# Performance work log

Hardware: AMD Instinct MI355X
Metric: run time of the kernel (lower is better)

Reference implementation:

```python
import jax, jax.numpy as jnp
import numpy as np

B, N, D, H = 8, 512, 512, 16
DH = D // H          # 32
HH = H // 2          # 8
DEG = 16
E = B * N * DEG      # 65536
LOG2 = float(np.log(2.0))


def _lin(key, fan_in, fan_out):
    k1, k2 = jax.random.split(key)
    s = 1.0 / np.sqrt(fan_in)
    W = jax.random.uniform(k1, (fan_in, fan_out), jnp.float32, -s, s)
    b = jax.random.uniform(k2, (fan_out,), jnp.float32, -s, s)
    return W, b


def setup_inputs() -> dict:
    key = jax.random.key(0)
    ks = jax.random.split(key, 12)
    inp = {}
    inp["key"] = jax.random.normal(ks[0], (B, N, D), jnp.float32)
    inp["value"] = jax.random.normal(ks[1], (B, N, D), jnp.float32)
    inp["query"] = jax.random.normal(ks[2], (B, N, D), jnp.float32)
    inp["mask"] = jnp.zeros((B, N, N), bool)
    inp["edge_feature"] = jax.random.normal(ks[3], (E, D), jnp.float32)
    # deterministic, collision-free (b,i,j) edge index: DEG neighbors per node
    inp["pair_b"] = jnp.repeat(jnp.arange(B, dtype=jnp.int32), N * DEG)
    i_idx = jnp.tile(jnp.repeat(jnp.arange(N, dtype=jnp.int32), DEG), B)
    inp["pair_i"] = i_idx
    inp["pair_j"] = (i_idx + 1 + jnp.tile(jnp.arange(DEG, dtype=jnp.int32), B * N)) % N
    inp["Wq"], inp["bq"] = _lin(ks[4], D, D)
    inp["Wk"], inp["bk"] = _lin(ks[5], D, D)
    inp["Wv"], inp["bv"] = _lin(ks[6], D, D)
    inp["Wo"], inp["bo"] = _lin(ks[7], D, D)
    inp["We1"], inp["be1"] = _lin(ks[8], D, D)
    inp["We2"], inp["be2"] = _lin(ks[9], D, D // 2)
    inp["Wu1"], inp["bu1"] = _lin(ks[10], 2 * D, D)
    inp["Wu2"], inp["bu2"] = _lin(ks[11], D, D)
    return inp


def reference(key, value, query, mask, edge_feature, pair_b, pair_i, pair_j,
              Wq, bq, Wk, bk, Wv, bv, Wo, bo,
              We1, be1, We2, be2, Wu1, bu1, Wu2, bu2):
    scale = 1.0 / np.sqrt(DH)

    def shape(x):  # (B,N,D) -> (B,H,N,DH)
        return x.reshape(B, N, H, DH).transpose(0, 2, 1, 3)

    k = shape(key @ Wk + bk)
    q = shape(query @ Wq + bq)
    v = shape(value @ Wv + bv)

    # ---- local, edge-indexed half (upper HH heads) ----
    ef = jax.nn.softplus(edge_feature @ We1 + be1) - LOG2  # SSP
    ef = (ef @ We2 + be2).reshape(E, HH, DH)
    k_loc = k[pair_b, HH:, pair_j] * ef                    # (E,HH,DH)
    q_loc = q[pair_b, HH:, pair_i] * scale                 # (E,HH,DH)
    scores_local = jnp.einsum('ehd,ehd->eh', q_loc, k_loc)  # (E,HH)
    score_expand = jnp.full((B, N, N, HH), -jnp.inf, scores_local.dtype)
    score_expand = score_expand.at[pair_b, pair_i, pair_j].set(scores_local)
    score_expand = score_expand.transpose(0, 3, 1, 2)      # (B,HH,N,N)
    valid = score_expand > -10000.0
    attn_local = jax.nn.softmax(jnp.where(valid, score_expand, -1e30), axis=-1)
    attn_local = jnp.where(valid, attn_local, 0.0)         # masked_fill
    local_ctx = attn_local @ v[:, HH:]                     # (B,HH,N,DH)

    # ---- global dense half (lower HH heads) ----
    score_g = jnp.einsum('bhqd,bhkd->bhqk', q[:, :HH] * scale, k[:, :HH])
    top_score = score_g[:, 0]                              # before masking, as in torch
    score_g = jnp.where(mask[:, None], -1e18, score_g)
    attn_g = jax.nn.softmax(score_g, axis=-1)
    global_ctx = attn_g @ v[:, :HH]                        # (B,HH,N,DH)

    ctx = jnp.concatenate([global_ctx, local_ctx], axis=-1)  # (B,HH,N,2*DH)
    ctx = ctx.transpose(0, 2, 1, 3).reshape(B, N, D)
    output = ctx @ Wo + bo                                 # (B,N,D)

    nf = jnp.concatenate([output[pair_b, pair_i], output[pair_b, pair_j]], axis=-1)
    eu = jax.nn.softplus(nf @ Wu1 + bu1) - LOG2
    edge_updated = eu @ Wu2 + bu2                          # (E,D)
    return output, top_score, edge_updated
```

## Files before the change

kernel.cpp:

```cpp
#include <hip/hip_runtime.h>
#include <math.h>

constexpr int Bc   = 8;
constexpr int Nc   = 512;
constexpr int Dc   = 512;
constexpr int HHc  = 8;
constexpr int DHc  = 32;
constexpr int DEGc = 16;
constexpr int Ec   = Bc * Nc * DEGc;
constexpr float LN2   = 0.69314718055994530942f;
constexpr float SCALE = 0.17677669529663688110f;

typedef unsigned short ushort_t;
typedef __attribute__((ext_vector_type(8))) short short8;
typedef __attribute__((ext_vector_type(4))) float f32x4;

__device__ __forceinline__ float splus_m_ln2(float x) {
    float t = __expf(-fabsf(x));
    return fmaxf(x, 0.0f) + __logf(1.0f + t) - LN2;
}

__device__ __forceinline__ ushort_t f2bf(float x) {
    union { float f; unsigned int u; } v; v.f = x;
    unsigned int r = (v.u + 0x7fffu + ((v.u >> 16) & 1u)) >> 16;
    return (ushort_t)r;
}
__device__ __forceinline__ float bf2f(ushort_t x) {
    union { unsigned int u; float f; } v; v.u = ((unsigned int)x) << 16;
    return v.f;
}

__device__ __forceinline__ void gload16(const ushort_t* g, ushort_t* l) {
    __builtin_amdgcn_global_load_lds(
        (const __attribute__((address_space(1))) void*)g,
        (__attribute__((address_space(3))) void*)l, 16, 0, 0);
}

template<int ACT, int GATHER, int OUTMODE, int K, int NOUT>
__global__ __launch_bounds__(256) void gemm_mfma(
    const ushort_t* __restrict__ A, const ushort_t* __restrict__ Bt,
    const float* __restrict__ bias, void* __restrict__ Cout,
    ushort_t* __restrict__ Cout2,
    const int* __restrict__ pb, const int* __restrict__ pi,
    const int* __restrict__ pj)
{
    __shared__ ushort_t As[2][128 * 32];
    __shared__ ushort_t Bs[2][128 * 32];

    const int t    = threadIdx.x;
    const int lane = t & 63;
    const int w    = t >> 6;
    const int wy   = w >> 1, wx = w & 1;
    const int rowBase = blockIdx.y * 128;
    const int colBase = blockIdx.x * 128;

    const int sm0 = t >> 2;
    const int kch = (t & 3) * 8;

    const ushort_t *a0i, *a0j = nullptr, *a1i, *a1j = nullptr;
    if (GATHER) {
        const int e0 = rowBase + sm0, e1 = rowBase + 64 + sm0;
        a0i = A + ((size_t)(pb[e0] * Nc + pi[e0])) * Dc;
        a0j = A + ((size_t)(pb[e0] * Nc + pj[e0])) * Dc;
        a1i = A + ((size_t)(pb[e1] * Nc + pi[e1])) * Dc;
        a1j = A + ((size_t)(pb[e1] * Nc + pj[e1])) * Dc;
    } else {
        a0i = A + (size_t)(rowBase + sm0) * K;
        a1i = A + (size_t)(rowBase + 64 + sm0) * K;
    }
    const ushort_t* b0 = Bt + (size_t)(colBase + sm0) * K;
    const ushort_t* b1 = Bt + (size_t)(colBase + 64 + sm0) * K;

    const int soff0 = w * 64 * 8;
    const int soff1 = (256 + w * 64) * 8;

    f32x4 acc[4][4];
    const f32x4 fz = {0.f, 0.f, 0.f, 0.f};
    #pragma unroll
    for (int i = 0; i < 4; ++i)
        #pragma unroll
        for (int j = 0; j < 4; ++j) acc[i][j] = fz;

    const int c16 = lane & 15;
    const int q16 = lane >> 4;

    auto STAGE = [&](int s, int kb) {
        const int k0 = kb << 5;
        const ushort_t *pa0, *pa1;
        if constexpr (GATHER) {
            if (kb < (Dc >> 5)) { pa0 = a0i + k0; pa1 = a1i + k0; }
            else                { pa0 = a0j + (k0 - Dc); pa1 = a1j + (k0 - Dc); }
        } else { pa0 = a0i + k0; pa1 = a1i + k0; }
        gload16(pa0 + kch, &As[s][soff0]);
        gload16(pa1 + kch, &As[s][soff1]);
        gload16(b0 + k0 + kch, &Bs[s][soff0]);
        gload16(b1 + k0 + kch, &Bs[s][soff1]);
    };

    auto COMPUTE = [&](int s) {
        short8 af[4], bfr[4];
        #pragma unroll
        for (int i = 0; i < 4; ++i)
            af[i] = *(const short8*)&As[s][(size_t)((wy * 64 + i * 16 + c16) * 32 + q16 * 8)];
        #pragma unroll
        for (int j = 0; j < 4; ++j)
            bfr[j] = *(const short8*)&Bs[s][(size_t)((wx * 64 + j * 16 + c16) * 32 + q16 * 8)];
        #pragma unroll
        for (int i = 0; i < 4; ++i)
            #pragma unroll
            for (int j = 0; j < 4; ++j)
                acc[i][j] = __builtin_amdgcn_mfma_f32_16x16x32_bf16(af[i], bfr[j], acc[i][j], 0, 0, 0);
    };

    constexpr int NKB = K >> 5;
    STAGE(0, 0);
    asm volatile("s_waitcnt vmcnt(0)" ::: "memory");
    __syncthreads();
    int cur = 0;
    #pragma unroll 2
    for (int kb = 0; kb < NKB; ++kb) {
        if (kb + 1 < NKB) STAGE(cur ^ 1, kb + 1);
        COMPUTE(cur);
        asm volatile("s_waitcnt vmcnt(0)" ::: "memory");
        __syncthreads();
        cur ^= 1;
    }

    #pragma unroll
    for (int j = 0; j < 4; ++j) {
        const int col = colBase + wx * 64 + j * 16 + c16;
        const float bv = bias[col];
        #pragma unroll
        for (int i = 0; i < 4; ++i) {
            const int row0 = rowBase + wy * 64 + i * 16 + q16 * 4;
            #pragma unroll
            for (int r = 0; r < 4; ++r) {
                float v = acc[i][j][r] + bv;
                if (ACT) v = splus_m_ln2(v);
                const size_t idx = (size_t)(row0 + r) * NOUT + col;
                if (OUTMODE == 1) {
                    ((ushort_t*)Cout)[idx] = f2bf(v);
                } else {
                    ((float*)Cout)[idx] = v;
                    if (OUTMODE == 2) Cout2[idx] = f2bf(v);
                }
            }
        }
    }
}

__global__ __launch_bounds__(256) void cvt_f32_bf16(
    const float* __restrict__ src, ushort_t* __restrict__ dst)
{
    const int i = blockIdx.x * 256 + threadIdx.x;
    float4 v = ((const float4*)src)[i];
    ushort4 o;
    o.x = f2bf(v.x); o.y = f2bf(v.y); o.z = f2bf(v.z); o.w = f2bf(v.w);
    ((ushort4*)dst)[i] = o;
}

__global__ void transpose_cvt(const float* __restrict__ W, ushort_t* __restrict__ Wt,
                              int K, int NOUT)
{
    __shared__ float tile[32][33];
    const int k0 = blockIdx.x * 32, n0 = blockIdx.y * 32;
    #pragma unroll
    for (int r = 0; r < 4; ++r)
        tile[threadIdx.y + r * 8][threadIdx.x] =
            W[(size_t)(k0 + threadIdx.y + r * 8) * NOUT + n0 + threadIdx.x];
    __syncthreads();
    #pragma unroll
    for (int r = 0; r < 4; ++r)
        Wt[(size_t)(n0 + threadIdx.y + r * 8) * K + k0 + threadIdx.x] =
            f2bf(tile[threadIdx.x][threadIdx.y + r * 8]);
}

__global__ __launch_bounds__(256) void global_attn(
    const float* __restrict__ qp, const float* __restrict__ kp,
    const float* __restrict__ vp, float* __restrict__ ctx,
    float* __restrict__ top)
{
    __shared__ float S[16 * 516];
    __shared__ float KV[128 * 36];
    __shared__ float Qs[16 * 36];

    const int t  = threadIdx.x;
    const int bh = blockIdx.y;
    const int b  = bh >> 3;
    const int h  = bh & (HHc - 1);
    const int q0 = blockIdx.x << 4;

    const size_t hb = ((size_t)b * Nc) * Dc + h * DHc;

    if (t < 128) {
        const int qr = t >> 3, off = (t & 7) << 2;
        float4 v = *(const float4*)&qp[hb + (size_t)(q0 + qr) * Dc + off];
        float* dst = &Qs[qr * 36 + off];
        dst[0] = v.x * SCALE; dst[1] = v.y * SCALE;
        dst[2] = v.z * SCALE; dst[3] = v.w * SCALE;
    }
    __syncthreads();

    const int q  = t >> 4;
    const int lj = t & 15;

    float qreg[32];
    #pragma unroll
    for (int d4 = 0; d4 < 8; ++d4) {
        float4 v = *(const float4*)&Qs[q * 36 + (d4 << 2)];
        qreg[(d4 << 2) + 0] = v.x; qreg[(d4 << 2) + 1] = v.y;
        qreg[(d4 << 2) + 2] = v.z; qreg[(d4 << 2) + 3] = v.w;
    }

    const int kr  = t >> 1;
    const int koff = (t & 1) << 4;
    for (int c = 0; c < 4; ++c) {
        __syncthreads();
        {
            const float* src = &kp[hb + (size_t)((c << 7) + kr) * Dc + koff];
            float* dst = &KV[kr * 36 + koff];
            *(float4*)&dst[0]  = *(const float4*)&src[0];
            *(float4*)&dst[4]  = *(const float4*)&src[4];
            *(float4*)&dst[8]  = *(const float4*)&src[8];
            *(float4*)&dst[12] = *(const float4*)&src[12];
        }
        __syncthreads();
        #pragma unroll
        for (int i = 0; i < 8; ++i) {
            const int k = lj + (i << 4);
            const float* krow = &KV[k * 36];
            float s0 = 0.f, s1 = 0.f, s2 = 0.f, s3 = 0.f;
            #pragma unroll
            for (int d4 = 0; d4 < 8; ++d4) {
                float4 kv4 = *(const float4*)&krow[d4 << 2];
                s0 += qreg[(d4 << 2) + 0] * kv4.x;
                s1 += qreg[(d4 << 2) + 1] * kv4.y;
                s2 += qreg[(d4 << 2) + 2] * kv4.z;
                s3 += qreg[(d4 << 2) + 3] * kv4.w;
            }
            S[q * 516 + (c << 7) + k] = (s0 + s1) + (s2 + s3);
        }
    }
    __syncthreads();

    if (h == 0) {
        float* trow = top + ((size_t)(b * Nc + q0)) * Nc;
        #pragma unroll
        for (int i = 0; i < 8; ++i) {
            const int f = (i << 8) + t;
            const int l = f << 2;
            const int r = l >> 9, k = l & 511;
            *(float4*)&trow[l] = *(const float4*)&S[r * 516 + k];
        }
        __syncthreads();
    }

    const int sbase = q * 516;
    float m = -1e30f;
    #pragma unroll
    for (int i = 0; i < 32; ++i)
        m = fmaxf(m, S[sbase + lj + (i << 4)]);
    #pragma unroll
    for (int off = 1; off < 16; off <<= 1)
        m = fmaxf(m, __shfl_xor(m, off, 64));
    float l = 0.f;
    #pragma unroll
    for (int i = 0; i < 32; ++i) {
        const int idx = sbase + lj + (i << 4);
        const float e = __expf(S[idx] - m);
        S[idx] = e;
        l += e;
    }
    #pragma unroll
    for (int off = 1; off < 16; off <<= 1)
        l += __shfl_xor(l, off, 64);
    const float inv = 1.0f / l;

    const int d2 = lj;
    float a00 = 0.f, a01 = 0.f, a10 = 0.f, a11 = 0.f;
    for (int c = 0; c < 4; ++c) {
        __syncthreads();
        {
            const float* src = &vp[hb + (size_t)((c << 7) + kr) * Dc + koff];
            float* dst = &KV[kr * 36 + koff];
            *(float4*)&dst[0]  = *(const float4*)&src[0];
            *(float4*)&dst[4]  = *(const float4*)&src[4];
            *(float4*)&dst[8]  = *(const float4*)&src[8];
            *(float4*)&dst[12] = *(const float4*)&src[12];
        }
        __syncthreads();
        const float* srow = &S[sbase + (c << 7)];
        #pragma unroll 8
        for (int k = 0; k < 128; k += 2) {
            const float w0 = srow[k];
            const float w1 = srow[k + 1];
            const float2 v0 = *(const float2*)&KV[k * 36 + (d2 << 1)];
            const float2 v1 = *(const float2*)&KV[(k + 1) * 36 + (d2 << 1)];
            a00 = fmaf(w0, v0.x, a00); a01 = fmaf(w0, v0.y, a01);
            a10 = fmaf(w1, v1.x, a10); a11 = fmaf(w1, v1.y, a11);
        }
    }
    float2 o;
    o.x = (a00 + a10) * inv;
    o.y = (a01 + a11) * inv;
    *(float2*)&ctx[((size_t)(b * Nc + q0 + q)) * Dc + (h << 6) + (d2 << 1)] = o;
}

__global__ __launch_bounds__(256) void local_scores(
    const float* __restrict__ qp, const float* __restrict__ kp,
    const ushort_t* __restrict__ ef2,
    const int* __restrict__ pb, const int* __restrict__ pi,
    const int* __restrict__ pj, float* __restrict__ sl)
{
    const int gid = blockIdx.x * 256 + threadIdx.x;
    const int h = gid & 7;
    const int e = gid >> 3;
    const int b = pb[e], i = pi[e], j = pj[e];
    const float* qrow = qp  + ((size_t)(b * Nc + i)) * Dc + (HHc + h) * DHc;
    const float* krow = kp  + ((size_t)(b * Nc + j)) * Dc + (HHc + h) * DHc;
    const ushort_t* erow = ef2 + (size_t)e * 256 + h * DHc;
    float s = 0.f;
    #pragma unroll
    for (int d4 = 0; d4 < 8; ++d4) {
        float4 qv = *(const float4*)&qrow[d4 << 2];
        float4 kv = *(const float4*)&krow[d4 << 2];
        ushort4 ev = *(const ushort4*)&erow[d4 << 2];
        s += qv.x * kv.x * bf2f(ev.x) + qv.y * kv.y * bf2f(ev.y)
           + qv.z * kv.z * bf2f(ev.z) + qv.w * kv.w * bf2f(ev.w);
    }
    sl[gid] = s * SCALE;
}

__global__ __launch_bounds__(256) void local_softmax(float* __restrict__ sl)
{
    const int gid = blockIdx.x * 256 + threadIdx.x;
    const int h  = gid & 7;
    const int bi = gid >> 3;
    float s[DEGc];
    float m = -1e30f;
    #pragma unroll
    for (int tt = 0; tt < DEGc; ++tt) {
        s[tt] = sl[(size_t)(bi * DEGc + tt) * 8 + h];
        m = fmaxf(m, s[tt]);
    }
    float l = 0.f;
    #pragma unroll
    for (int tt = 0; tt < DEGc; ++tt) { s[tt] = expf(s[tt] - m); l += s[tt]; }
    const float inv = 1.0f / l;
    #pragma unroll
    for (int tt = 0; tt < DEGc; ++tt)
        sl[(size_t)(bi * DEGc + tt) * 8 + h] = s[tt] * inv;
}

__global__ __launch_bounds__(256) void local_ctx_kernel(
    const float* __restrict__ vp, const float* __restrict__ sl,
    const int* __restrict__ pj, float* __restrict__ ctx)
{
    const int bi = blockIdx.x;
    const int t  = threadIdx.x;
    const int d  = t & 31;
    const int h  = t >> 5;
    __shared__ float a_s[DEGc][8];
    __shared__ int   jrow[DEGc];
    const int b = bi >> 9;
    if (t < DEGc) jrow[t] = pj[bi * DEGc + t];
    if (t < DEGc * 8) a_s[t >> 3][t & 7] = sl[(size_t)bi * (DEGc * 8) + t];
    __syncthreads();
    float acc = 0.f;
    #pragma unroll
    for (int tt = 0; tt < DEGc; ++tt) {
        const int j = jrow[tt];
        acc += a_s[tt][h] * vp[((size_t)(b * Nc + j)) * Dc + (HHc + h) * DHc + d];
    }
    ctx[(size_t)bi * Dc + (h << 6) + 32 + d] = acc;
}

extern "C" void kernel_launch(void* const* d_in, const int* in_sizes, int n_in,
                              void* d_out, int out_size, void* d_ws, size_t ws_size,
                              hipStream_t stream) {
    const float* key   = (const float*)d_in[0];
    const float* value = (const float*)d_in[1];
    const float* query = (const float*)d_in[2];
    const float* edge_feature = (const float*)d_in[4];
    const int* pb = (const int*)d_in[5];
    const int* pi = (const int*)d_in[6];
    const int* pj = (const int*)d_in[7];
    const float* Wq = (const float*)d_in[8];  const float* bq = (const float*)d_in[9];
    const float* Wk = (const float*)d_in[10]; const float* bk = (const float*)d_in[11];
    const float* Wv = (const float*)d_in[12]; const float* bv = (const float*)d_in[13];
    const float* Wo = (const float*)d_in[14]; const float* bo = (const float*)d_in[15];
    const float* We1 = (const float*)d_in[16]; const float* be1 = (const float*)d_in[17];
    const float* We2 = (const float*)d_in[18]; const float* be2 = (const float*)d_in[19];
    const float* Wu1 = (const float*)d_in[20]; const float* bu1 = (const float*)d_in[21];
    const float* Wu2 = (const float*)d_in[22]; const float* bu2 = (const float*)d_in[23];

    float* out  = (float*)d_out;
    float* top  = out + 2097152;
    float* eupd = out + 4194304;

    float* qp  = (float*)d_ws;
    float* kp  = qp + 2097152;
    float* vp  = kp + 2097152;
    float* ctx = vp + 2097152;
    float* sl  = ctx + 2097152;
    ushort_t* ef2b  = (ushort_t*)(sl + 524288);
    ushort_t* efb   = ef2b + 16777216;
    ushort_t* hidb  = efb + 33554432;
    ushort_t* outb  = hidb + 33554432;
    ushort_t* wt_e1 = outb + 2097152;
    ushort_t* wt_e2 = wt_e1 + 262144;
    ushort_t* wt_u1 = wt_e2 + 131072;
    ushort_t* wt_u2 = wt_u1 + 524288;

    ushort_t* wt_q = efb;
    ushort_t* wt_k = wt_q + 262144;
    ushort_t* wt_v = wt_k + 262144;
    ushort_t* wt_o = wt_v + 262144;
    ushort_t* qb   = wt_o + 262144;
    ushort_t* kb   = qb + 2097152;
    ushort_t* vb   = kb + 2097152;
    ushort_t* ctxb = vb + 2097152;

    dim3 blk(256);
    dim3 tblk(32, 8);

    transpose_cvt<<<dim3(16, 16), tblk, 0, stream>>>(We1, wt_e1, 512, 512);
    transpose_cvt<<<dim3(16, 8),  tblk, 0, stream>>>(We2, wt_e2, 512, 256);
    transpose_cvt<<<dim3(32, 16), tblk, 0, stream>>>(Wu1, wt_u1, 1024, 512);
    transpose_cvt<<<dim3(16, 16), tblk, 0, stream>>>(Wu2, wt_u2, 512, 512);
    cvt_f32_bf16<<<32768, blk, 0, stream>>>(edge_feature, efb);

    gemm_mfma<1, 0, 1, 512, 512><<<dim3(4, 512), blk, 0, stream>>>(efb, wt_e1, be1, hidb, nullptr, nullptr, nullptr, nullptr);
    gemm_mfma<0, 0, 1, 512, 256><<<dim3(2, 512), blk, 0, stream>>>(hidb, wt_e2, be2, ef2b, nullptr, nullptr, nullptr, nullptr);

    transpose_cvt<<<dim3(16, 16), tblk, 0, stream>>>(Wq, wt_q, 512, 512);
    transpose_cvt<<<dim3(16, 16), tblk, 0, stream>>>(Wk, wt_k, 512, 512);
    transpose_cvt<<<dim3(16, 16), tblk, 0, stream>>>(Wv, wt_v, 512, 512);
    transpose_cvt<<<dim3(16, 16), tblk, 0, stream>>>(Wo, wt_o, 512, 512);
    cvt_f32_bf16<<<2048, blk, 0, stream>>>(query, qb);
    cvt_f32_bf16<<<2048, blk, 0, stream>>>(key,   kb);
    cvt_f32_bf16<<<2048, blk, 0, stream>>>(value, vb);

    gemm_mfma<0, 0, 0, 512, 512><<<dim3(4, 32), blk, 0, stream>>>(qb, wt_q, bq, qp, nullptr, nullptr, nullptr, nullptr);
    gemm_mfma<0, 0, 0, 512, 512><<<dim3(4, 32), blk, 0, stream>>>(kb, wt_k, bk, kp, nullptr, nullptr, nullptr, nullptr);
    gemm_mfma<0, 0, 0, 512, 512><<<dim3(4, 32), blk, 0, stream>>>(vb, wt_v, bv, vp, nullptr, nullptr, nullptr, nullptr);

    global_attn<<<dim3(32, 64), blk, 0, stream>>>(qp, kp, vp, ctx, top);
    local_scores<<<2048, blk, 0, stream>>>(qp, kp, ef2b, pb, pi, pj, sl);
    local_softmax<<<128, blk, 0, stream>>>(sl);
    local_ctx_kernel<<<4096, blk, 0, stream>>>(vp, sl, pj, ctx);

    cvt_f32_bf16<<<2048, blk, 0, stream>>>(ctx, ctxb);
    gemm_mfma<0, 0, 2, 512, 512><<<dim3(4, 32), blk, 0, stream>>>(ctxb, wt_o, bo, out, outb, nullptr, nullptr, nullptr);

    gemm_mfma<1, 1, 1, 1024, 512><<<dim3(4, 512), blk, 0, stream>>>(outb, wt_u1, bu1, hidb, nullptr, pb, pi, pj);
    gemm_mfma<0, 0, 0, 512, 512><<<dim3(4, 512), blk, 0, stream>>>(hidb, wt_u2, bu2, eupd, nullptr, nullptr, nullptr, nullptr);
}
```

Before: 753.9 us.

## Factor edge-update GEMM through node projections, triple-buffer and swizzle GEMM LDS

The gathered edge-update first GEMM (E x 1024 x 512) is rewritten as two node-level GEMMs (output @ Wu1 top and bottom halves, 4096 rows each). A new elementwise kernel then gathers the two per-node results per edge, adds the bias and applies the shifted softplus. This cuts that stage's matmul work by roughly 16x at the cost of extra fp32 intermediates and a gather pass. Separately, the shared GEMM kernel moves to a 3-stage LDS pipeline with partial vmcnt waits and raw barriers, and XOR-swizzles the LDS layout to reduce bank conflicts. Fp32 accumulation of the split halves slightly changes rounding versus the bf16 gathered GEMM.

```diff
diff --git a/kernel.cpp b/kernel.cpp
--- a/kernel.cpp
+++ b/kernel.cpp
@@ -36,7 +36,7 @@
         (__attribute__((address_space(3))) void*)l, 16, 0, 0);
 }
 
-template<int ACT, int GATHER, int OUTMODE, int K, int NOUT>
+template<int ACT, int GATHER, int OUTMODE, int K, int NOUT, int BIAS = 1>
 __global__ __launch_bounds__(256) void gemm_mfma(
     const ushort_t* __restrict__ A, const ushort_t* __restrict__ Bt,
     const float* __restrict__ bias, void* __restrict__ Cout,
@@ -44,8 +44,8 @@
     const int* __restrict__ pb, const int* __restrict__ pi,
     const int* __restrict__ pj)
 {
-    __shared__ ushort_t As[2][128 * 32];
-    __shared__ ushort_t Bs[2][128 * 32];
+    __shared__ ushort_t As[3][128 * 32];
+    __shared__ ushort_t Bs[3][128 * 32];
 
     const int t    = threadIdx.x;
     const int lane = t & 63;
@@ -54,8 +54,8 @@
     const int rowBase = blockIdx.y * 128;
     const int colBase = blockIdx.x * 128;
 
-    const int sm0 = t >> 2;
-    const int kch = (t & 3) * 8;
+    const int sm0  = t >> 2;
+    const int kchs = (((t & 3) ^ ((t >> 2) & 3)) << 3);
 
     const ushort_t *a0i, *a0j = nullptr, *a1i, *a1j = nullptr;
     if (GATHER) {
@@ -83,6 +83,7 @@
 
     const int c16 = lane & 15;
     const int q16 = lane >> 4;
+    const int rdo = ((q16 ^ (c16 & 3)) << 3);
 
     auto STAGE = [&](int s, int kb) {
         const int k0 = kb << 5;
@@ -91,20 +92,20 @@
             if (kb < (Dc >> 5)) { pa0 = a0i + k0; pa1 = a1i + k0; }
             else                { pa0 = a0j + (k0 - Dc); pa1 = a1j + (k0 - Dc); }
         } else { pa0 = a0i + k0; pa1 = a1i + k0; }
-        gload16(pa0 + kch, &As[s][soff0]);
-        gload16(pa1 + kch, &As[s][soff1]);
-        gload16(b0 + k0 + kch, &Bs[s][soff0]);
-        gload16(b1 + k0 + kch, &Bs[s][soff1]);
+        gload16(pa0 + kchs, &As[s][soff0]);
+        gload16(pa1 + kchs, &As[s][soff1]);
+        gload16(b0 + k0 + kchs, &Bs[s][soff0]);
+        gload16(b1 + k0 + kchs, &Bs[s][soff1]);
     };
 
     auto COMPUTE = [&](int s) {
         short8 af[4], bfr[4];
         #pragma unroll
         for (int i = 0; i < 4; ++i)
-            af[i] = *(const short8*)&As[s][(size_t)((wy * 64 + i * 16 + c16) * 32 + q16 * 8)];
+            af[i] = *(const short8*)&As[s][(size_t)((wy * 64 + i * 16 + c16) * 32 + rdo)];
         #pragma unroll
         for (int j = 0; j < 4; ++j)
-            bfr[j] = *(const short8*)&Bs[s][(size_t)((wx * 64 + j * 16 + c16) * 32 + q16 * 8)];
+            bfr[j] = *(const short8*)&Bs[s][(size_t)((wx * 64 + j * 16 + c16) * 32 + rdo)];
         #pragma unroll
         for (int i = 0; i < 4; ++i)
             #pragma unroll
@@ -114,22 +115,24 @@
 
     constexpr int NKB = K >> 5;
     STAGE(0, 0);
+    STAGE(1, 1);
+    for (int kb = 0; kb < NKB - 2; ++kb) {
+        asm volatile("s_waitcnt vmcnt(4)" ::: "memory");
+        __builtin_amdgcn_s_barrier();
+        STAGE((kb + 2) % 3, kb + 2);
+        COMPUTE(kb % 3);
+    }
+    asm volatile("s_waitcnt vmcnt(4)" ::: "memory");
+    __builtin_amdgcn_s_barrier();
+    COMPUTE((NKB - 2) % 3);
     asm volatile("s_waitcnt vmcnt(0)" ::: "memory");
-    __syncthreads();
-    int cur = 0;
-    #pragma unroll 2
-    for (int kb = 0; kb < NKB; ++kb) {
-        if (kb + 1 < NKB) STAGE(cur ^ 1, kb + 1);
-        COMPUTE(cur);
-        asm volatile("s_waitcnt vmcnt(0)" ::: "memory");
-        __syncthreads();
-        cur ^= 1;
-    }
+    __builtin_amdgcn_s_barrier();
+    COMPUTE((NKB - 1) % 3);
 
     #pragma unroll
     for (int j = 0; j < 4; ++j) {
         const int col = colBase + wx * 64 + j * 16 + c16;
-        const float bv = bias[col];
+        const float bv = BIAS ? bias[col] : 0.0f;
         #pragma unroll
         for (int i = 0; i < 4; ++i) {
             const int row0 = rowBase + wy * 64 + i * 16 + q16 * 4;
@@ -147,6 +150,26 @@
             }
         }
     }
+}
+
+__global__ __launch_bounds__(256) void edge_u1_fuse(
+    const float* __restrict__ P1, const float* __restrict__ P2,
+    const float* __restrict__ bias,
+    const int* __restrict__ pb, const int* __restrict__ pi,
+    const int* __restrict__ pj, ushort_t* __restrict__ hid)
+{
+    const int e  = blockIdx.x * 2 + (threadIdx.x >> 7);
+    const int c4 = (threadIdx.x & 127) << 2;
+    const int b = pb[e], i = pi[e], j = pj[e];
+    const float4 a = *(const float4*)&P1[((size_t)(b * Nc + i)) * Dc + c4];
+    const float4 d = *(const float4*)&P2[((size_t)(b * Nc + j)) * Dc + c4];
+    const float4 bv = *(const float4*)&bias[c4];
+    ushort4 o;
+    o.x = f2bf(splus_m_ln2(a.x + d.x + bv.x));
+    o.y = f2bf(splus_m_ln2(a.y + d.y + bv.y));
+    o.z = f2bf(splus_m_ln2(a.z + d.z + bv.z));
+    o.w = f2bf(splus_m_ln2(a.w + d.w + bv.w));
+    *(ushort4*)&hid[(size_t)e * Dc + c4] = o;
 }
 
 __global__ __launch_bounds__(256) void cvt_f32_bf16(
@@ -420,13 +443,16 @@
     ushort_t* kb   = qb + 2097152;
     ushort_t* vb   = kb + 2097152;
     ushort_t* ctxb = vb + 2097152;
+    float* P1f = (float*)(ctxb + 2097152);
+    float* P2f = P1f + 2097152;
 
     dim3 blk(256);
     dim3 tblk(32, 8);
 
     transpose_cvt<<<dim3(16, 16), tblk, 0, stream>>>(We1, wt_e1, 512, 512);
     transpose_cvt<<<dim3(16, 8),  tblk, 0, stream>>>(We2, wt_e2, 512, 256);
-    transpose_cvt<<<dim3(32, 16), tblk, 0, stream>>>(Wu1, wt_u1, 1024, 512);
+    transpose_cvt<<<dim3(16, 16), tblk, 0, stream>>>(Wu1, wt_u1, 512, 512);
+    transpose_cvt<<<dim3(16, 16), tblk, 0, stream>>>(Wu1 + 512 * 512, wt_u1 + 262144, 512, 512);
     transpose_cvt<<<dim3(16, 16), tblk, 0, stream>>>(Wu2, wt_u2, 512, 512);
     cvt_f32_bf16<<<32768, blk, 0, stream>>>(edge_feature, efb);
 
@@ -453,6 +479,8 @@
     cvt_f32_bf16<<<2048, blk, 0, stream>>>(ctx, ctxb);
     gemm_mfma<0, 0, 2, 512, 512><<<dim3(4, 32), blk, 0, stream>>>(ctxb, wt_o, bo, out, outb, nullptr, nullptr, nullptr);
 
-    gemm_mfma<1, 1, 1, 1024, 512><<<dim3(4, 512), blk, 0, stream>>>(outb, wt_u1, bu1, hidb, nullptr, pb, pi, pj);
+    gemm_mfma<0, 0, 0, 512, 512, 0><<<dim3(4, 32), blk, 0, stream>>>(outb, wt_u1, bu1, P1f, nullptr, nullptr, nullptr, nullptr);
+    gemm_mfma<0, 0, 0, 512, 512, 0><<<dim3(4, 32), blk, 0, stream>>>(outb, wt_u1 + 262144, bu1, P2f, nullptr, nullptr, nullptr, nullptr);
+    edge_u1_fuse<<<32768, blk, 0, stream>>>(P1f, P2f, bu1, pb, pi, pj, hidb);
     gemm_mfma<0, 0, 0, 512, 512><<<dim3(4, 512), blk, 0, stream>>>(hidb, wt_u2, bu2, eupd, nullptr, nullptr, nullptr, nullptr);
 }
```

Measured after the change: 696.9 us. 1.08x faster.
